# Kernel tuning notes

Measured on AMD Instinct MI355X. Metric: run time of the kernel, lower is better.

Reference implementation:

```python
import jax, jax.numpy as jnp
import numpy as np
from jax import lax

NUM_CLASSES = 80
CONF = 0.05
IOU_T = 0.5
K_PER_CLASS = 100   # max_detections_per_class
MAX_DET = 100       # max_detections
BOX_VAR = np.array([0.1, 0.1, 0.2, 0.2], dtype=np.float32)


def make_anchors(H, W):
    """AnchorBox.get_anchors: [x, y, w, h] anchors for strides 8..128."""
    ratios = [0.5, 1.0, 2.0]
    scales = [2.0 ** 0, 2.0 ** (1.0 / 3.0), 2.0 ** (2.0 / 3.0)]
    strides = [8, 16, 32, 64, 128]
    areas = [32.0 ** 2, 64.0 ** 2, 128.0 ** 2, 256.0 ** 2, 512.0 ** 2]
    out = []
    for stride, area in zip(strides, areas):
        fh = int(np.ceil(H / stride)); fw = int(np.ceil(W / stride))
        dims = []
        for r in ratios:
            ah = np.sqrt(area / r); aw = area / ah
            for s in scales:
                dims.append([aw * s, ah * s])
        dims = np.array(dims, dtype=np.float32)              # [9,2]
        rx = (np.arange(fw, dtype=np.float32) + 0.5) * stride
        ry = (np.arange(fh, dtype=np.float32) + 0.5) * stride
        cx, cy = np.meshgrid(rx, ry)                         # [fh,fw]
        centers = np.stack([cx, cy], axis=-1)                # [fh,fw,2]
        centers = np.tile(centers[:, :, None, :], (1, 1, 9, 1))
        d = np.tile(dims[None, None, :, :], (fh, fw, 1, 1))
        out.append(np.concatenate([centers, d], axis=-1).reshape(-1, 4))
    return np.concatenate(out, axis=0).astype(np.float32)   # [N,4]


def _iou_matrix(boxes):
    # boxes: [K,4] corner format (x1,y1,x2,y2)
    lt = jnp.maximum(boxes[:, None, :2], boxes[None, :, :2])
    rb = jnp.minimum(boxes[:, None, 2:], boxes[None, :, 2:])
    inter = jnp.prod(jnp.clip(rb - lt, 0.0), axis=-1)
    area = jnp.prod(boxes[:, 2:] - boxes[:, :2], axis=-1)
    union = area[:, None] + area[None, :] - inter
    return inter / jnp.maximum(union, 1e-8)


def _decode(predictions, anchors):
    box_pred = predictions[..., :4] * jnp.asarray(BOX_VAR)
    xy = box_pred[..., :2] * anchors[:, 2:] + anchors[:, :2]
    wh = jnp.exp(box_pred[..., 2:]) * anchors[:, 2:]
    boxes = jnp.concatenate([xy - wh / 2.0, xy + wh / 2.0], axis=-1)  # [B,N,4] corners
    cls = jax.nn.sigmoid(predictions[..., 4:])                        # [B,N,C]
    return boxes, cls


def _nms_image(boxes, cls_scores):
    # boxes [N,4], cls_scores [N,C]
    rng = jnp.arange(K_PER_CLASS)

    def per_class(scores):  # [N]
        top_s, idx = lax.top_k(scores, K_PER_CLASS)
        cb = boxes[idx]                                      # [K,4]
        iou = lax.stop_gradient(_iou_matrix(cb))
        keep0 = top_s > CONF
        def body(i, keep):
            sup = keep[i] & (iou[i] > IOU_T) & (rng > i)
            return keep & (~sup)
        keep = lax.fori_loop(0, K_PER_CLASS, body, keep0)
        return cb, jnp.where(keep, top_s, -1.0)

    cboxes, cscores = jax.vmap(per_class)(cls_scores.T)      # [C,K,4], [C,K]
    cids = jnp.broadcast_to(jnp.arange(NUM_CLASSES, dtype=jnp.float32)[:, None],
                            (NUM_CLASSES, K_PER_CLASS))
    flat_s = cscores.reshape(-1)
    flat_b = cboxes.reshape(-1, 4)
    flat_c = cids.reshape(-1)
    fs, fi = lax.top_k(flat_s, MAX_DET)
    fb = flat_b[fi]
    fc = flat_c[fi]
    mask = fs > 0.0
    valid = jnp.sum(mask).astype(jnp.int32)
    return (jnp.where(mask[:, None], fb, 0.0),
            jnp.where(mask, fs, 0.0),
            jnp.where(mask, fc, 0.0),
            valid)


def setup_inputs() -> dict:
    key = jax.random.key(0)
    k1, k2 = jax.random.split(key)
    images = jax.random.normal(k1, (8, 512, 512, 3), dtype=jnp.float32)
    predictions = jax.random.normal(k2, (8, 49104, 84), dtype=jnp.float32)
    return {"images": images, "predictions": predictions}


def reference(images, predictions):
    H, W = images.shape[1], images.shape[2]
    anchors = jnp.asarray(make_anchors(H, W))                # [49104,4]
    boxes, cls = _decode(predictions, anchors)
    nmsed_boxes, nmsed_scores, nmsed_classes, valid = jax.vmap(_nms_image)(boxes, cls)
    return nmsed_boxes, nmsed_scores, nmsed_classes, valid
```

## Files before the change

kernel.cpp:

```cpp
#include <hip/hip_runtime.h>
#include <math.h>
#include <stdint.h>

#define NANCH 49104
#define NCLS 80
#define KSEL 100
#define NFLAT (NCLS * KSEL)
#define PREDC 84
#define NB 8
#define ECAP 128
#define BATF4 (NANCH * (PREDC / 4))
#define BPB 256
#define PCAP 16
#define LCAP 16
#define OCAP 64
#define FASTN 512
#define RMAX 8
#define CGRP 5
#define NCHUNK (NCLS / CGRP)
#define THRL 2.5f

struct DimsTable { float d[5][9][2]; };
struct KT { uint32_t key; int tie; };
typedef unsigned long long u64;

__device__ __forceinline__ uint32_t f2key(float f) {
    uint32_t u = __float_as_uint(f);
    return u ^ (uint32_t((int32_t)u >> 31) | 0x80000000u);
}
__device__ __forceinline__ float key2f(uint32_t k) {
    uint32_t u = (k & 0x80000000u) ? (k ^ 0x80000000u) : ~k;
    return __uint_as_float(u);
}
__device__ __forceinline__ float sigm(float x) { return 1.0f / (1.0f + expf(-x)); }

__device__ __forceinline__ void decode_box(const float4 pv, int n,
                                           const DimsTable& dt, float box[4]) {
    int lev, base, fw, stride;
    if (n < 36864)      { lev = 0; base = 0;     fw = 64; stride = 8;   }
    else if (n < 46080) { lev = 1; base = 36864; fw = 32; stride = 16;  }
    else if (n < 48384) { lev = 2; base = 46080; fw = 16; stride = 32;  }
    else if (n < 48960) { lev = 3; base = 48384; fw = 8;  stride = 64;  }
    else                { lev = 4; base = 48960; fw = 4;  stride = 128; }
    int i = n - base;
    int k = i % 9;
    int cell = i / 9;
    int xq = cell % fw, yq = cell / fw;
    float cx = ((float)xq + 0.5f) * (float)stride;
    float cy = ((float)yq + 0.5f) * (float)stride;
    float aw = dt.d[lev][k][0];
    float ah = dt.d[lev][k][1];
    float tx = __fmul_rn(pv.x, 0.1f);
    float ty = __fmul_rn(pv.y, 0.1f);
    float tw = __fmul_rn(pv.z, 0.2f);
    float th = __fmul_rn(pv.w, 0.2f);
    float px = __fadd_rn(__fmul_rn(tx, aw), cx);
    float py = __fadd_rn(__fmul_rn(ty, ah), cy);
    float pw = __fmul_rn(expf(tw), aw);
    float ph = __fmul_rn(expf(th), ah);
    float hw = __fmul_rn(pw, 0.5f);
    float hh = __fmul_rn(ph, 0.5f);
    box[0] = __fsub_rn(px, hw);
    box[1] = __fsub_rn(py, hh);
    box[2] = __fadd_rn(px, hw);
    box[3] = __fadd_rn(py, hh);
}

struct alignas(16) SelSh {
    int hist[2048];
    int suffix[256];
    uint32_t candKey[KSEL];
    int candIdx[KSEL];
    uint32_t eIdx[ECAP];
    uint32_t sKey[KSEL];
    int sIdx[KSEL];
    int cntG, cntE, krem, newkrem, digit, flast, rmin;
    uint32_t prefix, thrKey;
};

template <typename G>
__device__ int block_select(G get, int N, int K, SelSh& sh) {
    const int tid = threadIdx.x;
    int Ksel = (N < K) ? N : K;
    if (Ksel <= 0) return 0;

    if (N <= K) {
        if (tid < N) { KT e = get(tid); sh.candKey[tid] = e.key; sh.candIdx[tid] = e.tie; }
        __syncthreads();
        if (tid < N) {
            uint32_t mk = sh.candKey[tid]; int mi = sh.candIdx[tid];
            int rank = 0;
            for (int j = 0; j < N; ++j) {
                uint32_t kj = sh.candKey[j]; int ij = sh.candIdx[j];
                rank += (kj > mk) || (kj == mk && ij < mi);
            }
            sh.sKey[rank] = mk; sh.sIdx[rank] = mi;
        }
        __syncthreads();
        return Ksel;
    }

    if (tid == 0) { sh.krem = K; sh.prefix = 0; }
    for (int pass = 0; pass < 3; ++pass) {
        const int bins   = (pass == 2) ? 1024 : 2048;
        const int dshift = (pass == 0) ? 21 : (pass == 1 ? 10 : 0);
        const int fshift = (pass == 1) ? 21 : 10;
        const int dmask  = bins - 1;
        for (int j = tid; j < bins; j += 256) sh.hist[j] = 0;
        __syncthreads();
        const uint32_t pref = sh.prefix;
        for (int i = tid; i < N; i += 256) {
            uint32_t key = get(i).key;
            if (pass == 0) {
                atomicAdd(&sh.hist[(key >> dshift) & dmask], 1);
            } else if ((key >> fshift) == pref) {
                atomicAdd(&sh.hist[(key >> dshift) & dmask], 1);
            }
        }
        __syncthreads();
        const int cpb = bins / 256;
        const int base = tid * cpb;
        int lsum = 0;
        for (int j = 0; j < cpb; ++j) lsum += sh.hist[base + j];
        sh.suffix[tid] = lsum;
        __syncthreads();
        for (int off = 1; off < 256; off <<= 1) {
            int v = (tid + off < 256) ? sh.suffix[tid + off] : 0;
            __syncthreads();
            sh.suffix[tid] += v;
            __syncthreads();
        }
        {
            int cum = sh.suffix[tid] - lsum;
            const int krem = sh.krem;
            for (int j = cpb - 1; j >= 0; --j) {
                int cnt = sh.hist[base + j];
                if (cnt > 0 && cum < krem && cum + cnt >= krem) {
                    sh.digit = base + j;
                    sh.newkrem = krem - cum;
                }
                cum += cnt;
            }
        }
        __syncthreads();
        if (tid == 0) {
            sh.krem = sh.newkrem;
            if (pass == 0)      sh.prefix = (uint32_t)sh.digit;
            else if (pass == 1) sh.prefix = (sh.prefix << 11) | (uint32_t)sh.digit;
            else                sh.thrKey = (sh.prefix << 10) | (uint32_t)sh.digit;
        }
        __syncthreads();
    }

    if (tid == 0) { sh.cntG = 0; sh.cntE = 0; }
    __syncthreads();
    const uint32_t thr = sh.thrKey;
    for (int i = tid; i < N; i += 256) {
        KT e = get(i);
        if (e.key > thr) {
            int g = atomicAdd(&sh.cntG, 1);
            sh.candKey[g] = e.key; sh.candIdx[g] = e.tie;
        } else if (e.key == thr) {
            int idx = atomicAdd(&sh.cntE, 1);
            if (idx < ECAP) sh.eIdx[idx] = (uint32_t)e.tie;
        }
    }
    __syncthreads();
    const int need = sh.krem;
    const int nG = K - need;
    if (sh.cntE <= ECAP) {
        const int ce = sh.cntE;
        if (tid < ce) {
            uint32_t my = sh.eIdx[tid];
            int rank = 0;
            for (int j = 0; j < ce; ++j) rank += (sh.eIdx[j] < my);
            if (rank < need) { sh.candKey[nG + rank] = thr; sh.candIdx[nG + rank] = (int)my; }
        }
    } else {
        if (tid == 0) sh.flast = -1;
        __syncthreads();
        for (int t = 0; t < need; ++t) {
            if (tid == 0) sh.rmin = 0x7FFFFFFF;
            __syncthreads();
            const int fl = sh.flast;
            int lmin = 0x7FFFFFFF;
            for (int i = tid; i < N; i += 256) {
                KT e = get(i);
                if (e.key == thr && e.tie > fl) lmin = min(lmin, e.tie);
            }
            atomicMin(&sh.rmin, lmin);
            __syncthreads();
            if (tid == 0) { sh.candKey[nG + t] = thr; sh.candIdx[nG + t] = sh.rmin; sh.flast = sh.rmin; }
            __syncthreads();
        }
    }
    __syncthreads();
    if (tid < K) {
        uint32_t mk = sh.candKey[tid]; int mi = sh.candIdx[tid];
        int rank = 0;
        for (int j = 0; j < K; ++j) {
            uint32_t kj = sh.candKey[j]; int ij = sh.candIdx[j];
            rank += (kj > mk) || (kj == mk && ij < mi);
        }
        sh.sKey[rank] = mk; sh.sIdx[rank] = mi;
    }
    __syncthreads();
    return Ksel;
}

__global__ __launch_bounds__(256) void init_k(int* __restrict__ oflowCnt) {
    for (int x = threadIdx.x; x < NB * NCLS; x += 256) oflowCnt[x] = 0;
}

__device__ __forceinline__ void procf4(float4 p, int v, int b,
                                       int* lcnt, uint2 (*buck)[LCAP],
                                       int* oflowCnt, uint2* oflow) {
    uint32_t q = (uint32_t)v / 21u;
    uint32_t j = (uint32_t)v - q * 21u;
    if (j == 0u) return;
    bool c0 = p.x > THRL, c1 = p.y > THRL, c2 = p.z > THRL, c3 = p.w > THRL;
    if (!(c0 | c1 | c2 | c3)) return;
    uint32_t row = q - (uint32_t)b * (uint32_t)NANCH;
    int cbase = ((int)j - 1) * 4;
    float vv[4] = {p.x, p.y, p.z, p.w};
    bool pp[4] = {c0, c1, c2, c3};
#pragma unroll
    for (int k = 0; k < 4; ++k) {
        if (pp[k]) {
            int c = cbase + k;
            uint32_t key = f2key(sigm(vv[k]));
            int slot = atomicAdd(&lcnt[c], 1);
            if (slot < LCAP) {
                buck[c][slot] = make_uint2(key, row);
            } else {
                int bc = b * NCLS + c;
                int gs = atomicAdd(&oflowCnt[bc], 1);
                if (gs < OCAP) oflow[(size_t)bc * OCAP + gs] = make_uint2(key, row);
            }
        }
    }
}

__global__ __launch_bounds__(256) void cand_scan(const float4* __restrict__ predv,
                                                 uint2* __restrict__ cand2,
                                                 int* __restrict__ cnt2,
                                                 int* __restrict__ oflowCnt,
                                                 uint2* __restrict__ oflow) {
    __shared__ uint2 buck[NCLS][LCAP];
    __shared__ int lcnt[NCLS];

    const int tid = threadIdx.x;
    const int b = blockIdx.x / BPB;
    const int part = blockIdx.x - b * BPB;
    const int CH = (BATF4 + BPB - 1) / BPB;

    for (int j = tid; j < NCLS; j += 256) lcnt[j] = 0;
    __syncthreads();

    int s = b * BATF4 + part * CH;
    int e = b * BATF4 + BATF4;
    if (s + CH < e) e = s + CH;

    int v = s + tid;
    for (; v + 7 * 256 < e; v += 8 * 256) {
        float4 a0 = predv[v];
        float4 a1 = predv[v + 1 * 256];
        float4 a2 = predv[v + 2 * 256];
        float4 a3 = predv[v + 3 * 256];
        float4 a4 = predv[v + 4 * 256];
        float4 a5 = predv[v + 5 * 256];
        float4 a6 = predv[v + 6 * 256];
        float4 a7 = predv[v + 7 * 256];
        procf4(a0, v,           b, lcnt, buck, oflowCnt, oflow);
        procf4(a1, v + 1 * 256, b, lcnt, buck, oflowCnt, oflow);
        procf4(a2, v + 2 * 256, b, lcnt, buck, oflowCnt, oflow);
        procf4(a3, v + 3 * 256, b, lcnt, buck, oflowCnt, oflow);
        procf4(a4, v + 4 * 256, b, lcnt, buck, oflowCnt, oflow);
        procf4(a5, v + 5 * 256, b, lcnt, buck, oflowCnt, oflow);
        procf4(a6, v + 6 * 256, b, lcnt, buck, oflowCnt, oflow);
        procf4(a7, v + 7 * 256, b, lcnt, buck, oflowCnt, oflow);
    }
    for (; v < e; v += 256)
        procf4(predv[v], v, b, lcnt, buck, oflowCnt, oflow);
    __syncthreads();

    if (tid < NCLS) {
        int lc = lcnt[tid];
        if (lc > LCAP) lc = LCAP;
        cnt2[((size_t)b * NCLS + tid) * BPB + part] = lc;
    }
    for (int x = tid; x < NCLS * LCAP; x += 256) {
        int c = x >> 4;
        int k = x & (LCAP - 1);
        int lc = lcnt[c];
        if (lc > LCAP) lc = LCAP;
        if (k < lc)
            cand2[((size_t)(b * NCLS + c) * PCAP + k) * BPB + part] = buck[c][k];
    }
}

__global__ __launch_bounds__(256) void nms_sel(const float* __restrict__ pred,
                                               const uint2* __restrict__ cand2,
                                               const int* __restrict__ cnt2,
                                               const int* __restrict__ oflowCnt,
                                               const uint2* __restrict__ oflow,
                                               float* __restrict__ cls_boxes,
                                               uint32_t* __restrict__ posKeyC,
                                               uint32_t* __restrict__ posFlatC,
                                               int* __restrict__ posCntC,
                                               DimsTable dt) {
    __shared__ SelSh sh;
    __shared__ uint16_t prank[4][FASTN];
    __shared__ int wtot[4];
    __shared__ float sbox[KSEL][4];
    __shared__ float sarea[KSEL];
    __shared__ int sconf[KSEL];
    __shared__ alignas(16) uint32_t sup[KSEL][4];
    __shared__ uint32_t keepm[4];
    const int c = blockIdx.x;
    const int b = blockIdx.y;
    const int tid = threadIdx.x;
    const int bc = b * NCLS + c;
    const int lane = tid & 63;
    const int wid = tid >> 6;

    int myc = cnt2[(size_t)bc * BPB + tid];
    {
        int x = myc;
        for (int off = 1; off < 64; off <<= 1) {
            int y = __shfl_up(x, off);
            if (lane >= off) x += y;
        }
        if (lane == 63) wtot[wid] = x;
        __syncthreads();
        int base = 0;
#pragma unroll
        for (int w = 0; w < 4; ++w) if (w < wid) base += wtot[w];
        sh.suffix[tid] = base + x - myc;
    }
    const int excl = sh.suffix[tid];
    const int n0 = wtot[0] + wtot[1] + wtot[2] + wtot[3];
    const int of = oflowCnt[bc];
    const int n = n0 + of;

    if (n >= KSEL && n <= FASTN && of <= OCAP) {
        u64* list64 = (u64*)sh.hist;
        for (int k = 0; k < myc; ++k) {
            uint2 p = cand2[((size_t)bc * PCAP + k) * BPB + tid];
            list64[excl + k] = ((u64)p.x << 32) | (u64)(~p.y);
        }
        for (int x = tid; x < of; x += 256) {
            uint2 p = oflow[(size_t)bc * OCAP + x];
            list64[n0 + x] = ((u64)p.x << 32) | (u64)(~p.y);
        }
        __syncthreads();
        u64 cl[RMAX];
        int pr[RMAX];
#pragma unroll
        for (int r = 0; r < RMAX; ++r) {
            int i = r * 64 + lane;
            cl[r] = (i < n) ? list64[i] : 0xFFFFFFFFFFFFFFFFull;
            pr[r] = 0;
        }
        const int js = (wid * n) >> 2;
        const int je = ((wid + 1) * n) >> 2;
        int j = js;
        for (; j + 3 < je; j += 4) {
            u64 o0 = list64[j];
            u64 o1 = list64[j + 1];
            u64 o2 = list64[j + 2];
            u64 o3 = list64[j + 3];
#pragma unroll
            for (int r = 0; r < RMAX; ++r)
                pr[r] += (o0 > cl[r]) + (o1 > cl[r]) + (o2 > cl[r]) + (o3 > cl[r]);
        }
        for (; j < je; ++j) {
            u64 o = list64[j];
#pragma unroll
            for (int r = 0; r < RMAX; ++r) pr[r] += (o > cl[r]);
        }
#pragma unroll
        for (int r = 0; r < RMAX; ++r) {
            int i = r * 64 + lane;
            if (i < n) prank[wid][i] = (uint16_t)pr[r];
        }
        __syncthreads();
        for (int i = tid; i < n; i += 256) {
            int rank = (int)prank[0][i] + (int)prank[1][i]
                     + (int)prank[2][i] + (int)prank[3][i];
            if (rank < KSEL) {
                u64 e = list64[i];
                sh.sKey[rank] = (uint32_t)(e >> 32);
                sh.sIdx[rank] = (int)(~(uint32_t)e);
            }
        }
        __syncthreads();
    } else {
        const float* src = pred + (size_t)b * NANCH * PREDC + 4 + c;
        auto g = [src](int i) { KT e; e.key = f2key(sigm(src[(size_t)i * PREDC])); e.tie = i; return e; };
        block_select(g, NANCH, KSEL, sh);
    }

    for (int x = tid; x < KSEL * 4; x += 256) ((uint32_t*)sup)[x] = 0;
    if (tid < KSEL) {
        int ni = sh.sIdx[tid];
        float4 pv = reinterpret_cast<const float4*>(pred)[((size_t)b * NANCH + ni) * (PREDC / 4)];
        float bx[4]; decode_box(pv, ni, dt, bx);
        sbox[tid][0] = bx[0]; sbox[tid][1] = bx[1];
        sbox[tid][2] = bx[2]; sbox[tid][3] = bx[3];
        sarea[tid] = __fmul_rn(__fsub_rn(bx[2], bx[0]), __fsub_rn(bx[3], bx[1]));
        sconf[tid] = (key2f(sh.sKey[tid]) > 0.05f) ? 1 : 0;
    }
    __syncthreads();

    for (int pidx = tid; pidx < KSEL * KSEL; pidx += 256) {
        int i = pidx / KSEL;
        int jj = pidx - i * KSEL;
        if (jj > i && sconf[i] && sconf[jj]) {
            float x1 = fmaxf(sbox[i][0], sbox[jj][0]);
            float y1 = fmaxf(sbox[i][1], sbox[jj][1]);
            float x2 = fminf(sbox[i][2], sbox[jj][2]);
            float y2 = fminf(sbox[i][3], sbox[jj][3]);
            float iw = fmaxf(__fsub_rn(x2, x1), 0.0f);
            float ih = fmaxf(__fsub_rn(y2, y1), 0.0f);
            float inter = __fmul_rn(iw, ih);
            float uni = __fsub_rn(__fadd_rn(sarea[i], sarea[jj]), inter);
            if (__fdiv_rn(inter, fmaxf(uni, 1e-8f)) > 0.5f)
                atomicOr(&sup[i][jj >> 5], 1u << (jj & 31));
        }
    }
    __syncthreads();

    if (tid < 64) {
        const int l = tid;
        uint4 rowA = *reinterpret_cast<const uint4*>(sup[l]);
        int confA = sconf[l];
        uint4 rowB = make_uint4(0u, 0u, 0u, 0u);
        int confB = 0;
        if (l + 64 < KSEL) {
            rowB = *reinterpret_cast<const uint4*>(sup[l + 64]);
            confB = sconf[l + 64];
        }
        u64 mA = __ballot(confA != 0);
        u64 mB = __ballot(confB != 0);
        uint32_t k0 = (uint32_t)mA, k1 = (uint32_t)(mA >> 32);
        uint32_t k2 = (uint32_t)mB, k3 = (uint32_t)(mB >> 32);
        for (int i = 0; i < KSEL; ++i) {
            uint32_t w = (i < 32) ? k0 : (i < 64) ? k1 : (i < 96) ? k2 : k3;
            if ((w >> (i & 31)) & 1u) {
                uint32_t s0, s1, s2, s3;
                if (i < 64) {
                    s0 = __shfl(rowA.x, i); s1 = __shfl(rowA.y, i);
                    s2 = __shfl(rowA.z, i); s3 = __shfl(rowA.w, i);
                } else {
                    s0 = __shfl(rowB.x, i - 64); s1 = __shfl(rowB.y, i - 64);
                    s2 = __shfl(rowB.z, i - 64); s3 = __shfl(rowB.w, i - 64);
                }
                k0 &= ~s0; k1 &= ~s1; k2 &= ~s2; k3 &= ~s3;
            }
        }
        if (l == 0) {
            keepm[0] = k0; keepm[1] = k1; keepm[2] = k2; keepm[3] = k3;
            posCntC[bc] = __popc(k0) + __popc(k1) + __popc(k2) + __popc(k3);
        }
    }
    __syncthreads();

    if (tid < KSEL) {
        reinterpret_cast<float4*>(cls_boxes)[(size_t)b * NFLAT + c * KSEL + tid] =
            make_float4(sbox[tid][0], sbox[tid][1], sbox[tid][2], sbox[tid][3]);
        int w = tid >> 5, bit = tid & 31;
        if ((keepm[w] >> bit) & 1u) {
            int off = __popc(keepm[w] & ((bit == 0) ? 0u : ((1u << bit) - 1u)));
            for (int ww = 0; ww < w; ++ww) off += __popc(keepm[ww]);
            posKeyC[(size_t)bc * KSEL + off] = sh.sKey[tid];
            posFlatC[(size_t)bc * KSEL + off] = (uint32_t)(c * KSEL + tid);
        }
    }
}

__global__ __launch_bounds__(256) void chunk_sel(const uint32_t* __restrict__ posKeyC,
                                                 const uint32_t* __restrict__ posFlatC,
                                                 const int* __restrict__ posCntC,
                                                 u64* __restrict__ chunkOut,
                                                 int* __restrict__ chunkN) {
    __shared__ u64 list64[FASTN];
    __shared__ uint16_t prank[4][FASTN];
    __shared__ int csh[CGRP + 1];
    __shared__ u64 osel[KSEL];
    const int g = blockIdx.x;
    const int b = blockIdx.y;
    const int tid = threadIdx.x;
    const int lane = tid & 63;
    const int wid = tid >> 6;
    const int c0 = g * CGRP;

    if (tid == 0) {
        int acc = 0;
        for (int cc = 0; cc < CGRP; ++cc) {
            csh[cc] = acc;
            acc += posCntC[b * NCLS + c0 + cc];
        }
        csh[CGRP] = acc;
    }
    __syncthreads();
    const int n = csh[CGRP];

    for (int idx = tid; idx < CGRP * KSEL; idx += 256) {
        int cc = idx / KSEL;
        int k = idx - cc * KSEL;
        int base = csh[cc];
        if (k < csh[cc + 1] - base) {
            size_t sp = (size_t)(b * NCLS + c0 + cc) * KSEL + k;
            list64[base + k] = ((u64)posKeyC[sp] << 32) | (u64)(~posFlatC[sp]);
        }
    }
    __syncthreads();

    if (n > 0) {
        u64 cl[RMAX];
        int pr[RMAX];
#pragma unroll
        for (int r = 0; r < RMAX; ++r) {
            int i = r * 64 + lane;
            cl[r] = (i < n) ? list64[i] : 0xFFFFFFFFFFFFFFFFull;
            pr[r] = 0;
        }
        const int js = (wid * n) >> 2;
        const int je = ((wid + 1) * n) >> 2;
        int j = js;
        for (; j + 3 < je; j += 4) {
            u64 o0 = list64[j];
            u64 o1 = list64[j + 1];
            u64 o2 = list64[j + 2];
            u64 o3 = list64[j + 3];
#pragma unroll
            for (int r = 0; r < RMAX; ++r)
                pr[r] += (o0 > cl[r]) + (o1 > cl[r]) + (o2 > cl[r]) + (o3 > cl[r]);
        }
        for (; j < je; ++j) {
            u64 o = list64[j];
#pragma unroll
            for (int r = 0; r < RMAX; ++r) pr[r] += (o > cl[r]);
        }
#pragma unroll
        for (int r = 0; r < RMAX; ++r) {
            int i = r * 64 + lane;
            if (i < n) prank[wid][i] = (uint16_t)pr[r];
        }
        __syncthreads();
        for (int i = tid; i < n; i += 256) {
            int rank = (int)prank[0][i] + (int)prank[1][i]
                     + (int)prank[2][i] + (int)prank[3][i];
            if (rank < KSEL) osel[rank] = list64[i];
        }
    }
    __syncthreads();
    const int kn = (n < KSEL) ? n : KSEL;
    if (tid < kn)
        chunkOut[(size_t)(b * NCHUNK + g) * KSEL + tid] = osel[tid];
    if (tid == 0) chunkN[b * NCHUNK + g] = kn;
}

__global__ __launch_bounds__(256) void merge_sel(const u64* __restrict__ chunkOut,
                                                 const int* __restrict__ chunkN,
                                                 const float* __restrict__ cls_boxes,
                                                 float* __restrict__ out) {
    __shared__ u64 lst[NCHUNK][KSEL];
    __shared__ int ln[NCHUNK];
    __shared__ u64 osel[KSEL];
    __shared__ int okcnt;
    const int b = blockIdx.x;
    const int tid = threadIdx.x;

    if (tid < NCHUNK) ln[tid] = chunkN[b * NCHUNK + tid];
    if (tid == 0) okcnt = 0;
    __syncthreads();
    for (int x = tid; x < NCHUNK * KSEL; x += 256) {
        int g = x / KSEL;
        int k = x - g * KSEL;
        lst[g][k] = (k < ln[g]) ? chunkOut[(size_t)(b * NCHUNK + g) * KSEL + k] : 0ull;
    }
    __syncthreads();

    if (tid < 64) {
        const int l = tid;
        u64 h = (l < NCHUNK) ? lst[l][0] : 0ull;
        int p = 0;
        for (int r = 0; r < KSEL; ++r) {
            u64 m = h;
#pragma unroll
            for (int off = 8; off >= 1; off >>= 1) {
                u64 o = __shfl_xor(m, off);
                if (o > m) m = o;
            }
            if (l < NCHUNK && h == m && m != 0ull) {
                ++p;
                h = (p < ln[l]) ? lst[l][p] : 0ull;
            }
            if (l == 0) osel[r] = m;
        }
    }
    __syncthreads();

    if (tid < KSEL) {
        u64 e = osel[tid];
        float4 ob = make_float4(0.f, 0.f, 0.f, 0.f);
        float sv = 0.f, cv = 0.f;
        if (e != 0ull) {
            uint32_t key = (uint32_t)(e >> 32);
            int flat = (int)(~(uint32_t)e);
            sv = key2f(key);
            ob = reinterpret_cast<const float4*>(cls_boxes)[(size_t)b * NFLAT + flat];
            cv = (float)(flat / KSEL);
            atomicAdd(&okcnt, 1);
        }
        reinterpret_cast<float4*>(out)[(size_t)b * KSEL + tid] = ob;
        out[NB * KSEL * 4 + b * KSEL + tid] = sv;
        out[NB * KSEL * 5 + b * KSEL + tid] = cv;
    }
    __syncthreads();
    if (tid == 0) out[NB * KSEL * 6 + b] = (float)okcnt;
}

extern "C" void kernel_launch(void* const* d_in, const int* in_sizes, int n_in,
                              void* d_out, int out_size, void* d_ws, size_t ws_size,
                              hipStream_t stream) {
    const float* pred = (const float*)d_in[1];
    float* out = (float*)d_out;

    DimsTable dt;
    const double areasd[5] = {1024.0, 4096.0, 16384.0, 65536.0, 262144.0};
    const double ratios[3] = {0.5, 1.0, 2.0};
    const double scales[3] = {1.0, pow(2.0, 1.0 / 3.0), pow(2.0, 2.0 / 3.0)};
    for (int l = 0; l < 5; ++l)
        for (int ri = 0; ri < 3; ++ri) {
            double ah = sqrt(areasd[l] / ratios[ri]);
            double aw = areasd[l] / ah;
            for (int si = 0; si < 3; ++si) {
                dt.d[l][ri * 3 + si][0] = (float)(aw * scales[si]);
                dt.d[l][ri * 3 + si][1] = (float)(ah * scales[si]);
            }
        }

    char* wsb = (char*)d_ws;
    int* oflowCnt = (int*)wsb;
    int* posCntC  = oflowCnt + NB * NCLS;
    int* chunkNb  = posCntC + NB * NCLS;
    uint2* oflow  = (uint2*)(wsb + 16384);
    uint2* cand2  = oflow + (size_t)NB * NCLS * OCAP;
    int* cnt2     = (int*)(cand2 + (size_t)NB * NCLS * PCAP * BPB);
    float* cls_boxes = (float*)(cnt2 + (size_t)NB * NCLS * BPB);
    uint32_t* posKeyC  = (uint32_t*)(cls_boxes + (size_t)NB * NFLAT * 4);
    uint32_t* posFlatC = posKeyC + (size_t)NB * NFLAT;
    u64* chunkOut = (u64*)(posFlatC + (size_t)NB * NFLAT);

    init_k<<<1, 256, 0, stream>>>(oflowCnt);

    cand_scan<<<NB * BPB, 256, 0, stream>>>(reinterpret_cast<const float4*>(pred),
                                            cand2, cnt2, oflowCnt, oflow);

    dim3 gb(NCLS, NB);
    nms_sel<<<gb, 256, 0, stream>>>(pred, cand2, cnt2, oflowCnt, oflow,
                                    cls_boxes, posKeyC, posFlatC, posCntC, dt);

    dim3 gc(NCHUNK, NB);
    chunk_sel<<<gc, 256, 0, stream>>>(posKeyC, posFlatC, posCntC, chunkOut, chunkNb);

    merge_sel<<<NB, 256, 0, stream>>>(chunkOut, chunkNb, cls_boxes, out);
}
```

Before: 118.5 us.

## Fuse pipeline stages into one cooperative kernel with grid syncs

```diff
diff --git a/kernel.cpp b/kernel.cpp
--- a/kernel.cpp
+++ b/kernel.cpp
@@ -1,6 +1,9 @@
 #include <hip/hip_runtime.h>
+#include <hip/hip_cooperative_groups.h>
 #include <math.h>
 #include <stdint.h>
+
+namespace cg = cooperative_groups;
 
 #define NANCH 49104
 #define NCLS 80
@@ -10,14 +13,13 @@
 #define NB 8
 #define ECAP 128
 #define BATF4 (NANCH * (PREDC / 4))
-#define BPB 256
-#define PCAP 16
-#define LCAP 16
-#define OCAP 64
+#define BPB 128
+#define PCAP 24
 #define FASTN 512
 #define RMAX 8
 #define CGRP 5
 #define NCHUNK (NCLS / CGRP)
+#define GRID_TOTAL (NB * BPB)
 #define THRL 2.5f
 
 struct DimsTable { float d[5][9][2]; };
@@ -77,6 +79,34 @@
     int cntG, cntE, krem, newkrem, digit, flast, rmin;
     uint32_t prefix, thrKey;
 };
+struct alignas(16) ScanSh {
+    uint2 buck[NCLS][PCAP];
+    int lcnt[NCLS];
+};
+struct alignas(16) NmsSh {
+    SelSh sel;
+    uint16_t prank[4][FASTN];
+    int wtot[4];
+    int oflAny;
+    float sbox[KSEL][4];
+    float sarea[KSEL];
+    int sconf[KSEL];
+    alignas(16) uint32_t sup[KSEL][4];
+    uint32_t keepm[4];
+};
+struct alignas(16) ChunkSh {
+    u64 list64[FASTN];
+    uint16_t prank[4][FASTN];
+    int csh[CGRP + 1];
+    u64 osel[KSEL];
+};
+struct alignas(16) MergeSh {
+    u64 lst[NCHUNK][KSEL];
+    int ln[NCHUNK];
+    u64 osel[KSEL];
+    int okcnt;
+};
+union AllSh { ScanSh scan; NmsSh nms; ChunkSh chunk; MergeSh merge; };
 
 template <typename G>
 __device__ int block_select(G get, int N, int K, SelSh& sh) {
@@ -111,11 +141,8 @@
         const uint32_t pref = sh.prefix;
         for (int i = tid; i < N; i += 256) {
             uint32_t key = get(i).key;
-            if (pass == 0) {
-                atomicAdd(&sh.hist[(key >> dshift) & dmask], 1);
-            } else if ((key >> fshift) == pref) {
-                atomicAdd(&sh.hist[(key >> dshift) & dmask], 1);
-            }
+            if (pass == 0) atomicAdd(&sh.hist[(key >> dshift) & dmask], 1);
+            else if ((key >> fshift) == pref) atomicAdd(&sh.hist[(key >> dshift) & dmask], 1);
         }
         __syncthreads();
         const int cpb = bins / 256;
@@ -208,13 +235,8 @@
     return Ksel;
 }
 
-__global__ __launch_bounds__(256) void init_k(int* __restrict__ oflowCnt) {
-    for (int x = threadIdx.x; x < NB * NCLS; x += 256) oflowCnt[x] = 0;
-}
-
 __device__ __forceinline__ void procf4(float4 p, int v, int b,
-                                       int* lcnt, uint2 (*buck)[LCAP],
-                                       int* oflowCnt, uint2* oflow) {
+                                       int* lcnt, uint2 (*buck)[PCAP]) {
     uint32_t q = (uint32_t)v / 21u;
     uint32_t j = (uint32_t)v - q * 21u;
     if (j == 0u) return;
@@ -230,31 +252,21 @@
             int c = cbase + k;
             uint32_t key = f2key(sigm(vv[k]));
             int slot = atomicAdd(&lcnt[c], 1);
-            if (slot < LCAP) {
-                buck[c][slot] = make_uint2(key, row);
-            } else {
-                int bc = b * NCLS + c;
-                int gs = atomicAdd(&oflowCnt[bc], 1);
-                if (gs < OCAP) oflow[(size_t)bc * OCAP + gs] = make_uint2(key, row);
-            }
-        }
-    }
-}
-
-__global__ __launch_bounds__(256) void cand_scan(const float4* __restrict__ predv,
-                                                 uint2* __restrict__ cand2,
-                                                 int* __restrict__ cnt2,
-                                                 int* __restrict__ oflowCnt,
-                                                 uint2* __restrict__ oflow) {
-    __shared__ uint2 buck[NCLS][LCAP];
-    __shared__ int lcnt[NCLS];
-
+            if (slot < PCAP) buck[c][slot] = make_uint2(key, row);
+        }
+    }
+}
+
+__device__ void phase_scan(const float4* __restrict__ predv,
+                           uint2* __restrict__ cand2, int* __restrict__ cnt2,
+                           int blk, char* smemc) {
+    ScanSh& sh = *reinterpret_cast<ScanSh*>(smemc);
     const int tid = threadIdx.x;
-    const int b = blockIdx.x / BPB;
-    const int part = blockIdx.x - b * BPB;
+    const int b = blk / BPB;
+    const int part = blk - b * BPB;
     const int CH = (BATF4 + BPB - 1) / BPB;
 
-    for (int j = tid; j < NCLS; j += 256) lcnt[j] = 0;
+    for (int j = tid; j < NCLS; j += 256) sh.lcnt[j] = 0;
     __syncthreads();
 
     int s = b * BATF4 + part * CH;
@@ -271,87 +283,77 @@
         float4 a5 = predv[v + 5 * 256];
         float4 a6 = predv[v + 6 * 256];
         float4 a7 = predv[v + 7 * 256];
-        procf4(a0, v,           b, lcnt, buck, oflowCnt, oflow);
-        procf4(a1, v + 1 * 256, b, lcnt, buck, oflowCnt, oflow);
-        procf4(a2, v + 2 * 256, b, lcnt, buck, oflowCnt, oflow);
-        procf4(a3, v + 3 * 256, b, lcnt, buck, oflowCnt, oflow);
-        procf4(a4, v + 4 * 256, b, lcnt, buck, oflowCnt, oflow);
-        procf4(a5, v + 5 * 256, b, lcnt, buck, oflowCnt, oflow);
-        procf4(a6, v + 6 * 256, b, lcnt, buck, oflowCnt, oflow);
-        procf4(a7, v + 7 * 256, b, lcnt, buck, oflowCnt, oflow);
+        procf4(a0, v,           b, sh.lcnt, sh.buck);
+        procf4(a1, v + 1 * 256, b, sh.lcnt, sh.buck);
+        procf4(a2, v + 2 * 256, b, sh.lcnt, sh.buck);
+        procf4(a3, v + 3 * 256, b, sh.lcnt, sh.buck);
+        procf4(a4, v + 4 * 256, b, sh.lcnt, sh.buck);
+        procf4(a5, v + 5 * 256, b, sh.lcnt, sh.buck);
+        procf4(a6, v + 6 * 256, b, sh.lcnt, sh.buck);
+        procf4(a7, v + 7 * 256, b, sh.lcnt, sh.buck);
     }
     for (; v < e; v += 256)
-        procf4(predv[v], v, b, lcnt, buck, oflowCnt, oflow);
+        procf4(predv[v], v, b, sh.lcnt, sh.buck);
     __syncthreads();
 
     if (tid < NCLS) {
-        int lc = lcnt[tid];
-        if (lc > LCAP) lc = LCAP;
-        cnt2[((size_t)b * NCLS + tid) * BPB + part] = lc;
-    }
-    for (int x = tid; x < NCLS * LCAP; x += 256) {
-        int c = x >> 4;
-        int k = x & (LCAP - 1);
-        int lc = lcnt[c];
-        if (lc > LCAP) lc = LCAP;
+        int lc = sh.lcnt[tid];
+        int val = (lc > PCAP) ? (PCAP | 0x10000) : lc;
+        cnt2[((size_t)b * NCLS + tid) * BPB + part] = val;
+    }
+    for (int x = tid; x < NCLS * PCAP; x += 256) {
+        int c = x / PCAP;
+        int k = x - c * PCAP;
+        int lc = sh.lcnt[c];
+        if (lc > PCAP) lc = PCAP;
         if (k < lc)
-            cand2[((size_t)(b * NCLS + c) * PCAP + k) * BPB + part] = buck[c][k];
-    }
-}
-
-__global__ __launch_bounds__(256) void nms_sel(const float* __restrict__ pred,
-                                               const uint2* __restrict__ cand2,
-                                               const int* __restrict__ cnt2,
-                                               const int* __restrict__ oflowCnt,
-                                               const uint2* __restrict__ oflow,
-                                               float* __restrict__ cls_boxes,
-                                               uint32_t* __restrict__ posKeyC,
-                                               uint32_t* __restrict__ posFlatC,
-                                               int* __restrict__ posCntC,
-                                               DimsTable dt) {
-    __shared__ SelSh sh;
-    __shared__ uint16_t prank[4][FASTN];
-    __shared__ int wtot[4];
-    __shared__ float sbox[KSEL][4];
-    __shared__ float sarea[KSEL];
-    __shared__ int sconf[KSEL];
-    __shared__ alignas(16) uint32_t sup[KSEL][4];
-    __shared__ uint32_t keepm[4];
-    const int c = blockIdx.x;
-    const int b = blockIdx.y;
+            cand2[((size_t)(b * NCLS + c) * PCAP + k) * BPB + part] = sh.buck[c][k];
+    }
+}
+
+__device__ void phase_nms(const float* __restrict__ pred,
+                          const uint2* __restrict__ cand2,
+                          const int* __restrict__ cnt2,
+                          float* __restrict__ cls_boxes,
+                          uint32_t* __restrict__ posKeyC,
+                          uint32_t* __restrict__ posFlatC,
+                          int* __restrict__ posCntC,
+                          const DimsTable& dt, int blk, char* smemc) {
+    NmsSh& sh = *reinterpret_cast<NmsSh*>(smemc);
+    const int b = blk / NCLS;
+    const int c = blk - b * NCLS;
     const int tid = threadIdx.x;
     const int bc = b * NCLS + c;
     const int lane = tid & 63;
     const int wid = tid >> 6;
 
-    int myc = cnt2[(size_t)bc * BPB + tid];
-    {
-        int x = myc;
-        for (int off = 1; off < 64; off <<= 1) {
-            int y = __shfl_up(x, off);
-            if (lane >= off) x += y;
-        }
-        if (lane == 63) wtot[wid] = x;
-        __syncthreads();
-        int base = 0;
-#pragma unroll
-        for (int w = 0; w < 4; ++w) if (w < wid) base += wtot[w];
-        sh.suffix[tid] = base + x - myc;
-    }
-    const int excl = sh.suffix[tid];
-    const int n0 = wtot[0] + wtot[1] + wtot[2] + wtot[3];
-    const int of = oflowCnt[bc];
-    const int n = n0 + of;
-
-    if (n >= KSEL && n <= FASTN && of <= OCAP) {
-        u64* list64 = (u64*)sh.hist;
-        for (int k = 0; k < myc; ++k) {
-            uint2 p = cand2[((size_t)bc * PCAP + k) * BPB + tid];
-            list64[excl + k] = ((u64)p.x << 32) | (u64)(~p.y);
-        }
-        for (int x = tid; x < of; x += 256) {
-            uint2 p = oflow[(size_t)bc * OCAP + x];
-            list64[n0 + x] = ((u64)p.x << 32) | (u64)(~p.y);
+    if (tid == 0) sh.oflAny = 0;
+    __syncthreads();
+
+    int myc = 0;
+    if (tid < BPB) {
+        int vv = cnt2[(size_t)bc * BPB + tid];
+        myc = vv & 0xFFFF;
+        if (vv >> 16) atomicOr(&sh.oflAny, 1);
+    }
+    int x = myc;
+    for (int off = 1; off < 64; off <<= 1) {
+        int y = __shfl_up(x, off);
+        if (lane >= off) x += y;
+    }
+    if (lane == 63 && wid < 2) sh.wtot[wid] = x;
+    __syncthreads();
+    const int excl = (wid == 0) ? (x - myc) : (sh.wtot[0] + x - myc);
+    const int n = sh.wtot[0] + sh.wtot[1];
+    const bool fb = (sh.oflAny != 0) || (n < KSEL) || (n > FASTN);
+
+    if (!fb) {
+        u64* list64 = (u64*)sh.sel.hist;
+        if (tid < BPB) {
+            for (int k = 0; k < myc; ++k) {
+                uint2 p = cand2[((size_t)bc * PCAP + k) * BPB + tid];
+                list64[excl + k] = ((u64)p.x << 32) | (u64)(~p.y);
+            }
         }
         __syncthreads();
         u64 cl[RMAX];
@@ -382,64 +384,64 @@
 #pragma unroll
         for (int r = 0; r < RMAX; ++r) {
             int i = r * 64 + lane;
-            if (i < n) prank[wid][i] = (uint16_t)pr[r];
+            if (i < n) sh.prank[wid][i] = (uint16_t)pr[r];
         }
         __syncthreads();
         for (int i = tid; i < n; i += 256) {
-            int rank = (int)prank[0][i] + (int)prank[1][i]
-                     + (int)prank[2][i] + (int)prank[3][i];
+            int rank = (int)sh.prank[0][i] + (int)sh.prank[1][i]
+                     + (int)sh.prank[2][i] + (int)sh.prank[3][i];
             if (rank < KSEL) {
                 u64 e = list64[i];
-                sh.sKey[rank] = (uint32_t)(e >> 32);
-                sh.sIdx[rank] = (int)(~(uint32_t)e);
+                sh.sel.sKey[rank] = (uint32_t)(e >> 32);
+                sh.sel.sIdx[rank] = (int)(~(uint32_t)e);
             }
         }
         __syncthreads();
     } else {
         const float* src = pred + (size_t)b * NANCH * PREDC + 4 + c;
         auto g = [src](int i) { KT e; e.key = f2key(sigm(src[(size_t)i * PREDC])); e.tie = i; return e; };
-        block_select(g, NANCH, KSEL, sh);
-    }
-
-    for (int x = tid; x < KSEL * 4; x += 256) ((uint32_t*)sup)[x] = 0;
+        block_select(g, NANCH, KSEL, sh.sel);
+    }
+
+    for (int xx = tid; xx < KSEL * 4; xx += 256) ((uint32_t*)sh.sup)[xx] = 0;
     if (tid < KSEL) {
-        int ni = sh.sIdx[tid];
+        int ni = sh.sel.sIdx[tid];
         float4 pv = reinterpret_cast<const float4*>(pred)[((size_t)b * NANCH + ni) * (PREDC / 4)];
         float bx[4]; decode_box(pv, ni, dt, bx);
-        sbox[tid][0] = bx[0]; sbox[tid][1] = bx[1];
-        sbox[tid][2] = bx[2]; sbox[tid][3] = bx[3];
-        sarea[tid] = __fmul_rn(__fsub_rn(bx[2], bx[0]), __fsub_rn(bx[3], bx[1]));
-        sconf[tid] = (key2f(sh.sKey[tid]) > 0.05f) ? 1 : 0;
+        sh.sbox[tid][0] = bx[0]; sh.sbox[tid][1] = bx[1];
+        sh.sbox[tid][2] = bx[2]; sh.sbox[tid][3] = bx[3];
+        sh.sarea[tid] = __fmul_rn(__fsub_rn(bx[2], bx[0]), __fsub_rn(bx[3], bx[1]));
+        sh.sconf[tid] = (key2f(sh.sel.sKey[tid]) > 0.05f) ? 1 : 0;
     }
     __syncthreads();
 
     for (int pidx = tid; pidx < KSEL * KSEL; pidx += 256) {
         int i = pidx / KSEL;
         int jj = pidx - i * KSEL;
-        if (jj > i && sconf[i] && sconf[jj]) {
-            float x1 = fmaxf(sbox[i][0], sbox[jj][0]);
-            float y1 = fmaxf(sbox[i][1], sbox[jj][1]);
-            float x2 = fminf(sbox[i][2], sbox[jj][2]);
-            float y2 = fminf(sbox[i][3], sbox[jj][3]);
+        if (jj > i && sh.sconf[i] && sh.sconf[jj]) {
+            float x1 = fmaxf(sh.sbox[i][0], sh.sbox[jj][0]);
+            float y1 = fmaxf(sh.sbox[i][1], sh.sbox[jj][1]);
+            float x2 = fminf(sh.sbox[i][2], sh.sbox[jj][2]);
+            float y2 = fminf(sh.sbox[i][3], sh.sbox[jj][3]);
             float iw = fmaxf(__fsub_rn(x2, x1), 0.0f);
             float ih = fmaxf(__fsub_rn(y2, y1), 0.0f);
             float inter = __fmul_rn(iw, ih);
-            float uni = __fsub_rn(__fadd_rn(sarea[i], sarea[jj]), inter);
+            float uni = __fsub_rn(__fadd_rn(sh.sarea[i], sh.sarea[jj]), inter);
             if (__fdiv_rn(inter, fmaxf(uni, 1e-8f)) > 0.5f)
-                atomicOr(&sup[i][jj >> 5], 1u << (jj & 31));
+                atomicOr(&sh.sup[i][jj >> 5], 1u << (jj & 31));
         }
     }
     __syncthreads();
 
     if (tid < 64) {
         const int l = tid;
-        uint4 rowA = *reinterpret_cast<const uint4*>(sup[l]);
-        int confA = sconf[l];
+        uint4 rowA = *reinterpret_cast<const uint4*>(sh.sup[l]);
+        int confA = sh.sconf[l];
         uint4 rowB = make_uint4(0u, 0u, 0u, 0u);
         int confB = 0;
         if (l + 64 < KSEL) {
-            rowB = *reinterpret_cast<const uint4*>(sup[l + 64]);
-            confB = sconf[l + 64];
+            rowB = *reinterpret_cast<const uint4*>(sh.sup[l + 64]);
+            confB = sh.sconf[l + 64];
         }
         u64 mA = __ballot(confA != 0);
         u64 mB = __ballot(confB != 0);
@@ -460,7 +462,7 @@
             }
         }
         if (l == 0) {
-            keepm[0] = k0; keepm[1] = k1; keepm[2] = k2; keepm[3] = k3;
+            sh.keepm[0] = k0; sh.keepm[1] = k1; sh.keepm[2] = k2; sh.keepm[3] = k3;
             posCntC[bc] = __popc(k0) + __popc(k1) + __popc(k2) + __popc(k3);
         }
     }
@@ -468,28 +470,25 @@
 
     if (tid < KSEL) {
         reinterpret_cast<float4*>(cls_boxes)[(size_t)b * NFLAT + c * KSEL + tid] =
-            make_float4(sbox[tid][0], sbox[tid][1], sbox[tid][2], sbox[tid][3]);
+            make_float4(sh.sbox[tid][0], sh.sbox[tid][1], sh.sbox[tid][2], sh.sbox[tid][3]);
         int w = tid >> 5, bit = tid & 31;
-        if ((keepm[w] >> bit) & 1u) {
-            int off = __popc(keepm[w] & ((bit == 0) ? 0u : ((1u << bit) - 1u)));
-            for (int ww = 0; ww < w; ++ww) off += __popc(keepm[ww]);
-            posKeyC[(size_t)bc * KSEL + off] = sh.sKey[tid];
+        if ((sh.keepm[w] >> bit) & 1u) {
+            int off = __popc(sh.keepm[w] & ((bit == 0) ? 0u : ((1u << bit) - 1u)));
+            for (int ww = 0; ww < w; ++ww) off += __popc(sh.keepm[ww]);
+            posKeyC[(size_t)bc * KSEL + off] = sh.sel.sKey[tid];
             posFlatC[(size_t)bc * KSEL + off] = (uint32_t)(c * KSEL + tid);
         }
     }
 }
 
-__global__ __launch_bounds__(256) void chunk_sel(const uint32_t* __restrict__ posKeyC,
-                                                 const uint32_t* __restrict__ posFlatC,
-                                                 const int* __restrict__ posCntC,
-                                                 u64* __restrict__ chunkOut,
-                                                 int* __restrict__ chunkN) {
-    __shared__ u64 list64[FASTN];
-    __shared__ uint16_t prank[4][FASTN];
-    __shared__ int csh[CGRP + 1];
-    __shared__ u64 osel[KSEL];
-    const int g = blockIdx.x;
-    const int b = blockIdx.y;
+__device__ void phase_chunk(const uint32_t* __restrict__ posKeyC,
+                            const uint32_t* __restrict__ posFlatC,
+                            const int* __restrict__ posCntC,
+                            u64* __restrict__ chunkOut, int* __restrict__ chunkN,
+                            int blk, char* smemc) {
+    ChunkSh& sh = *reinterpret_cast<ChunkSh*>(smemc);
+    const int b = blk / NCHUNK;
+    const int g = blk - b * NCHUNK;
     const int tid = threadIdx.x;
     const int lane = tid & 63;
     const int wid = tid >> 6;
@@ -498,21 +497,21 @@
     if (tid == 0) {
         int acc = 0;
         for (int cc = 0; cc < CGRP; ++cc) {
-            csh[cc] = acc;
+            sh.csh[cc] = acc;
             acc += posCntC[b * NCLS + c0 + cc];
         }
-        csh[CGRP] = acc;
-    }
-    __syncthreads();
-    const int n = csh[CGRP];
+        sh.csh[CGRP] = acc;
+    }
+    __syncthreads();
+    const int n = sh.csh[CGRP];
 
     for (int idx = tid; idx < CGRP * KSEL; idx += 256) {
         int cc = idx / KSEL;
         int k = idx - cc * KSEL;
-        int base = csh[cc];
-        if (k < csh[cc + 1] - base) {
+        int base = sh.csh[cc];
+        if (k < sh.csh[cc + 1] - base) {
             size_t sp = (size_t)(b * NCLS + c0 + cc) * KSEL + k;
-            list64[base + k] = ((u64)posKeyC[sp] << 32) | (u64)(~posFlatC[sp]);
+            sh.list64[base + k] = ((u64)posKeyC[sp] << 32) | (u64)(~posFlatC[sp]);
         }
     }
     __syncthreads();
@@ -523,69 +522,66 @@
 #pragma unroll
         for (int r = 0; r < RMAX; ++r) {
             int i = r * 64 + lane;
-            cl[r] = (i < n) ? list64[i] : 0xFFFFFFFFFFFFFFFFull;
+            cl[r] = (i < n) ? sh.list64[i] : 0xFFFFFFFFFFFFFFFFull;
             pr[r] = 0;
         }
         const int js = (wid * n) >> 2;
         const int je = ((wid + 1) * n) >> 2;
         int j = js;
         for (; j + 3 < je; j += 4) {
-            u64 o0 = list64[j];
-            u64 o1 = list64[j + 1];
-            u64 o2 = list64[j + 2];
-            u64 o3 = list64[j + 3];
+            u64 o0 = sh.list64[j];
+            u64 o1 = sh.list64[j + 1];
+            u64 o2 = sh.list64[j + 2];
+            u64 o3 = sh.list64[j + 3];
 #pragma unroll
             for (int r = 0; r < RMAX; ++r)
                 pr[r] += (o0 > cl[r]) + (o1 > cl[r]) + (o2 > cl[r]) + (o3 > cl[r]);
         }
         for (; j < je; ++j) {
-            u64 o = list64[j];
+            u64 o = sh.list64[j];
 #pragma unroll
             for (int r = 0; r < RMAX; ++r) pr[r] += (o > cl[r]);
         }
 #pragma unroll
         for (int r = 0; r < RMAX; ++r) {
             int i = r * 64 + lane;
-            if (i < n) prank[wid][i] = (uint16_t)pr[r];
+            if (i < n) sh.prank[wid][i] = (uint16_t)pr[r];
         }
         __syncthreads();
         for (int i = tid; i < n; i += 256) {
-            int rank = (int)prank[0][i] + (int)prank[1][i]
-                     + (int)prank[2][i] + (int)prank[3][i];
-            if (rank < KSEL) osel[rank] = list64[i];
+            int rank = (int)sh.prank[0][i] + (int)sh.prank[1][i]
+                     + (int)sh.prank[2][i] + (int)sh.prank[3][i];
+            if (rank < KSEL) sh.osel[rank] = sh.list64[i];
         }
     }
     __syncthreads();
     const int kn = (n < KSEL) ? n : KSEL;
     if (tid < kn)
-        chunkOut[(size_t)(b * NCHUNK + g) * KSEL + tid] = osel[tid];
+        chunkOut[(size_t)(b * NCHUNK + g) * KSEL + tid] = sh.osel[tid];
     if (tid == 0) chunkN[b * NCHUNK + g] = kn;
 }
 
-__global__ __launch_bounds__(256) void merge_sel(const u64* __restrict__ chunkOut,
-                                                 const int* __restrict__ chunkN,
-                                                 const float* __restrict__ cls_boxes,
-                                                 float* __restrict__ out) {
-    __shared__ u64 lst[NCHUNK][KSEL];
-    __shared__ int ln[NCHUNK];
-    __shared__ u64 osel[KSEL];
-    __shared__ int okcnt;
-    const int b = blockIdx.x;
+__device__ void phase_merge(const u64* __restrict__ chunkOut,
+                            const int* __restrict__ chunkN,
+                            const float* __restrict__ cls_boxes,
+                            float* __restrict__ out, int blk, char* smemc) {
+    MergeSh& sh = *reinterpret_cast<MergeSh*>(smemc);
+    const int b = blk;
     const int tid = threadIdx.x;
 
-    if (tid < NCHUNK) ln[tid] = chunkN[b * NCHUNK + tid];
-    if (tid == 0) okcnt = 0;
+    if (tid < NCHUNK) sh.ln[tid] = chunkN[b * NCHUNK + tid];
+    if (tid == 0) sh.okcnt = 0;
     __syncthreads();
     for (int x = tid; x < NCHUNK * KSEL; x += 256) {
         int g = x / KSEL;
         int k = x - g * KSEL;
-        lst[g][k] = (k < ln[g]) ? chunkOut[(size_t)(b * NCHUNK + g) * KSEL + k] : 0ull;
+        sh.lst[g][k] = (k < sh.ln[g]) ? chunkOut[(size_t)(b * NCHUNK + g) * KSEL + k] : 0ull;
     }
     __syncthreads();
 
     if (tid < 64) {
         const int l = tid;
-        u64 h = (l < NCHUNK) ? lst[l][0] : 0ull;
+        u64 h = (l < NCHUNK) ? sh.lst[l][0] : 0ull;
         int p = 0;
         for (int r = 0; r < KSEL; ++r) {
             u64 m = h;
@@ -596,15 +592,15 @@
             }
             if (l < NCHUNK && h == m && m != 0ull) {
                 ++p;
-                h = (p < ln[l]) ? lst[l][p] : 0ull;
-            }
-            if (l == 0) osel[r] = m;
+                h = (p < sh.ln[l]) ? sh.lst[l][p] : 0ull;
+            }
+            if (l == 0) sh.osel[r] = m;
         }
     }
     __syncthreads();
 
     if (tid < KSEL) {
-        u64 e = osel[tid];
+        u64 e = sh.osel[tid];
         float4 ob = make_float4(0.f, 0.f, 0.f, 0.f);
         float sv = 0.f, cv = 0.f;
         if (e != 0ull) {
@@ -613,20 +609,72 @@
             sv = key2f(key);
             ob = reinterpret_cast<const float4*>(cls_boxes)[(size_t)b * NFLAT + flat];
             cv = (float)(flat / KSEL);
-            atomicAdd(&okcnt, 1);
+            atomicAdd(&sh.okcnt, 1);
         }
         reinterpret_cast<float4*>(out)[(size_t)b * KSEL + tid] = ob;
         out[NB * KSEL * 4 + b * KSEL + tid] = sv;
         out[NB * KSEL * 5 + b * KSEL + tid] = cv;
     }
     __syncthreads();
-    if (tid == 0) out[NB * KSEL * 6 + b] = (float)okcnt;
+    if (tid == 0) out[NB * KSEL * 6 + b] = (float)sh.okcnt;
+}
+
+__global__ __launch_bounds__(256, 4) void fused_all(
+    const float4* predv, const float* pred, uint2* cand2, int* cnt2,
+    float* cls_boxes, uint32_t* posKeyC, uint32_t* posFlatC, int* posCntC,
+    u64* chunkOut, int* chunkN, float* out, DimsTable dt) {
+    __shared__ AllSh smem;
+    cg::grid_group grid = cg::this_grid();
+    const int blk = blockIdx.x;
+
+    phase_scan(predv, cand2, cnt2, blk, (char*)&smem);
+    __threadfence();
+    grid.sync();
+    if (blk < NB * NCLS)
+        phase_nms(pred, cand2, cnt2, cls_boxes, posKeyC, posFlatC, posCntC, dt,
+                  blk, (char*)&smem);
+    __threadfence();
+    grid.sync();
+    if (blk < NB * NCHUNK)
+        phase_chunk(posKeyC, posFlatC, posCntC, chunkOut, chunkN, blk, (char*)&smem);
+    __threadfence();
+    grid.sync();
+    if (blk < NB)
+        phase_merge(chunkOut, chunkN, cls_boxes, out, blk, (char*)&smem);
+}
+
+__global__ __launch_bounds__(256) void scan_k(const float4* predv, uint2* cand2,
+                                              int* cnt2) {
+    __shared__ ScanSh smem;
+    phase_scan(predv, cand2, cnt2, blockIdx.x, (char*)&smem);
+}
+__global__ __launch_bounds__(256) void nms_k(const float* pred, const uint2* cand2,
+                                             const int* cnt2, float* cls_boxes,
+                                             uint32_t* posKeyC, uint32_t* posFlatC,
+                                             int* posCntC, DimsTable dt) {
+    __shared__ NmsSh smem;
+    phase_nms(pred, cand2, cnt2, cls_boxes, posKeyC, posFlatC, posCntC, dt,
+              blockIdx.x, (char*)&smem);
+}
+__global__ __launch_bounds__(256) void chunk_k(const uint32_t* posKeyC,
+                                               const uint32_t* posFlatC,
+                                               const int* posCntC, u64* chunkOut,
+                                               int* chunkN) {
+    __shared__ ChunkSh smem;
+    phase_chunk(posKeyC, posFlatC, posCntC, chunkOut, chunkN, blockIdx.x,
+                (char*)&smem);
+}
+__global__ __launch_bounds__(256) void merge_k(const u64* chunkOut, const int* chunkN,
+                                               const float* cls_boxes, float* out) {
+    __shared__ MergeSh smem;
+    phase_merge(chunkOut, chunkN, cls_boxes, out, blockIdx.x, (char*)&smem);
 }
 
 extern "C" void kernel_launch(void* const* d_in, const int* in_sizes, int n_in,
                               void* d_out, int out_size, void* d_ws, size_t ws_size,
                               hipStream_t stream) {
     const float* pred = (const float*)d_in[1];
+    const float4* predv = reinterpret_cast<const float4*>(pred);
     float* out = (float*)d_out;
 
     DimsTable dt;
@@ -644,28 +692,39 @@
         }
 
     char* wsb = (char*)d_ws;
-    int* oflowCnt = (int*)wsb;
-    int* posCntC  = oflowCnt + NB * NCLS;
-    int* chunkNb  = posCntC + NB * NCLS;
-    uint2* oflow  = (uint2*)(wsb + 16384);
-    uint2* cand2  = oflow + (size_t)NB * NCLS * OCAP;
-    int* cnt2     = (int*)(cand2 + (size_t)NB * NCLS * PCAP * BPB);
+    int* posCntC = (int*)wsb;
+    int* chunkNb = posCntC + NB * NCLS;
+    uint2* cand2 = (uint2*)(wsb + 16384);
+    int* cnt2 = (int*)(cand2 + (size_t)NB * NCLS * PCAP * BPB);
     float* cls_boxes = (float*)(cnt2 + (size_t)NB * NCLS * BPB);
-    uint32_t* posKeyC  = (uint32_t*)(cls_boxes + (size_t)NB * NFLAT * 4);
+    uint32_t* posKeyC = (uint32_t*)(cls_boxes + (size_t)NB * NFLAT * 4);
     uint32_t* posFlatC = posKeyC + (size_t)NB * NFLAT;
     u64* chunkOut = (u64*)(posFlatC + (size_t)NB * NFLAT);
 
-    init_k<<<1, 256, 0, stream>>>(oflowCnt);
-
-    cand_scan<<<NB * BPB, 256, 0, stream>>>(reinterpret_cast<const float4*>(pred),
-                                            cand2, cnt2, oflowCnt, oflow);
-
-    dim3 gb(NCLS, NB);
-    nms_sel<<<gb, 256, 0, stream>>>(pred, cand2, cnt2, oflowCnt, oflow,
-                                    cls_boxes, posKeyC, posFlatC, posCntC, dt);
-
-    dim3 gc(NCHUNK, NB);
-    chunk_sel<<<gc, 256, 0, stream>>>(posKeyC, posFlatC, posCntC, chunkOut, chunkNb);
-
-    merge_sel<<<NB, 256, 0, stream>>>(chunkOut, chunkNb, cls_boxes, out);
-}
+    int maxb = 0;
+    hipError_t qerr = hipOccupancyMaxActiveBlocksPerMultiprocessor(
+        &maxb, reinterpret_cast<const void*>(&fused_all), 256, 0);
+    bool coop_ok = (qerr == hipSuccess) && (maxb >= 4);
+
+    if (coop_ok) {
+        void* args[] = {(void*)&predv, (void*)&pred, (void*)&cand2, (void*)&cnt2,
+                        (void*)&cls_boxes, (void*)&posKeyC, (void*)&posFlatC,
+                        (void*)&posCntC, (void*)&chunkOut, (void*)&chunkNb,
+                        (void*)&out, (void*)&dt};
+        hipError_t lerr = hipLaunchCooperativeKernel(
+            reinterpret_cast<void*>(&fused_all), dim3(GRID_TOTAL), dim3(256),
+            args, 0, stream);
+        if (lerr != hipSuccess) {
+            (void)hipGetLastError();
+            coop_ok = false;
+        }
+    }
+    if (!coop_ok) {
+        scan_k<<<GRID_TOTAL, 256, 0, stream>>>(predv, cand2, cnt2);
+        nms_k<<<NB * NCLS, 256, 0, stream>>>(pred, cand2, cnt2, cls_boxes,
+                                             posKeyC, posFlatC, posCntC, dt);
+        chunk_k<<<NB * NCHUNK, 256, 0, stream>>>(posKeyC, posFlatC, posCntC,
+                                                 chunkOut, chunkNb);
+        merge_k<<<NB, 256, 0, stream>>>(chunkOut, chunkNb, cls_boxes, out);
+    }
+}
```

New measurement: 122.7 us. 3.6% more time.
